# Optimization experiments

Measured on AMD Instinct MI355X. Metric: run time of the kernel, lower is better.

## Reference

```python
import jax, jax.numpy as jnp
import numpy as np

EPS = 1e-08
BASE_CR = 0.5
MIN_CR = 0.1


def _layernorm(h, g, b, eps=1e-5):
    m = jnp.mean(h, axis=-1, keepdims=True)
    v = jnp.mean((h - m) ** 2, axis=-1, keepdims=True)
    return (h - m) * jax.lax.rsqrt(v + eps) * g + b


def _normalize(h, eps=1e-12):
    n = jnp.sqrt(jnp.sum(h * h, axis=-1, keepdims=True))
    return h / jnp.maximum(n, eps)


def _conv1d(h, w, b):
    # h: [B,S,D], w: [K,I,O] (WIO), cross-correlation, SAME padding (torch Conv1d padding=1, k=3)
    y = jax.lax.conv_general_dilated(h, w, window_strides=(1,), padding='SAME',
                                     dimension_numbers=('NWC', 'WIO', 'NWC'))
    return y + b


def setup_inputs() -> dict:
    key = jax.random.key(0)
    ks = jax.random.split(key, 8)
    V, L, D, B, S = 50257, 2048, 1024, 8, 2048
    inp = {
        'x': jax.random.randint(ks[0], (B, S), 0, V),
        'token_emb': jax.random.normal(ks[1], (V, D), jnp.float32) * 0.02,
        'pos_emb': jax.random.normal(ks[2], (L, D), jnp.float32) * 0.02,
        'conv1_w': jax.random.normal(ks[3], (3, D, D), jnp.float32) * 0.025,
        'conv1_b': jnp.zeros((D,), jnp.float32),
        'conv2_w': jax.random.normal(ks[4], (3, D, D), jnp.float32) * 0.025,
        'conv2_b': jnp.zeros((D,), jnp.float32),
        'proj_w': jax.random.normal(ks[5], (D, D), jnp.float32) * 0.03,
        'proj_b': jnp.zeros((D,), jnp.float32),
        'ph_w': jax.random.normal(ks[6], (D, D), jnp.float32) * 0.03,
        'ph_b': jnp.zeros((D,), jnp.float32),
        'ln_g': jnp.ones((D,), jnp.float32),
        'ln_b': jnp.zeros((D,), jnp.float32),
    }
    return inp


def reference(x, token_emb, pos_emb, conv1_w, conv1_b, conv2_w, conv2_b,
              proj_w, proj_b, ph_w, ph_b, ln_g, ln_b):
    B, S = x.shape
    # token + position embedding
    h = token_emb[x] + pos_emb[:S][None, :, :]                 # [B,S,D]
    # two conv1d + gelu (exact erf, matching torch F.gelu default)
    h = jax.nn.gelu(_conv1d(h, conv1_w, conv1_b), approximate=False)
    h = jax.nn.gelu(_conv1d(h, conv2_w, conv2_b), approximate=False)
    h = _layernorm(h, ln_g, ln_b)
    # dropout is identity in eval mode
    # S is a power of two -> next_power_of_two(S) == S, no padding
    x_fft = jnp.fft.fft(h, axis=1)                              # [B,S,D] complex64
    magnitude = jnp.abs(x_fft)
    thresh = 0.1 * jnp.max(magnitude, axis=1, keepdims=True)
    complexity = jnp.mean((magnitude > thresh).astype(jnp.float32), axis=(1, 2))  # [B]
    cr = jnp.clip(BASE_CR * (1.0 - complexity), MIN_CR, 1.0)
    N = jnp.clip((cr * S).astype(jnp.int32), 1, S)              # [B] kept coefficients
    # vectorized ragged masking (replaces per-sample python loop/scatter)
    mask = (jnp.arange(S)[None, :] < N[:, None]).astype(jnp.float32)   # [B,S]
    x_fft_c = x_fft * mask[:, :, None]
    x_ifft_raw = jnp.fft.ifft(x_fft_c, n=S, axis=1).real        # [B,S,D]
    proj_out = x_ifft_raw @ proj_w + proj_b
    x_ifft = _layernorm(proj_out, ln_g, ln_b)
    recon_target = proj_out                                     # same proj of same ifft
    # loss
    cos_sim = jnp.sum(_normalize(x_ifft) * _normalize(recon_target), axis=-1)
    cos_sim = jnp.clip(cos_sim, -1.0 + EPS, 1.0 - EPS)
    d = x_ifft - recon_target
    l1 = jnp.where(jnp.abs(d) < 1.0, 0.5 * d * d, jnp.abs(d) - 0.5)    # smooth_l1, beta=1
    proj_x = x_ifft @ ph_w + ph_b
    proj_t = recon_target @ ph_w + ph_b
    sem = jnp.mean((_normalize(proj_x) - _normalize(proj_t)) ** 2, axis=-1)  # [B,S]
    combined = 0.6 * jnp.mean(1.0 - cos_sim) + 0.2 * jnp.mean(l1, axis=-1) + 0.2 * sem
    loss = jnp.sum(combined * mask) / (jnp.sum(mask) + EPS)
    return (x_ifft, loss)
```

## Files before the change

### kernel.cpp

```cpp
#include <hip/hip_runtime.h>
#include <math.h>

#define S_LEN 2048
#define D_DIM 1024
#define B_BATCH 8
#define R_ROWS (B_BATCH * S_LEN)
#define BD_ROWS (B_BATCH * D_DIM)
#define PAD_ROWS 2050

typedef unsigned short u16;
typedef unsigned int u32;
typedef __attribute__((ext_vector_type(8))) short bf16x8;
typedef __attribute__((ext_vector_type(4))) float f32x4;

__device__ __forceinline__ u16 f2bf(float f) {
    u32 x = __float_as_uint(f);
    u32 r = (x + 0x7fffu + ((x >> 16) & 1u)) >> 16;
    return (u16)r;
}
__device__ __forceinline__ float bf2f(u16 u) {
    return __uint_as_float(((u32)u) << 16);
}
__device__ __forceinline__ float gelu_exact(float x) {
    return 0.5f * x * (1.0f + erff(x * 0.70710678118654752f));
}
__device__ __forceinline__ int dr4(int v) {
    v = __brev((unsigned)v) >> 22;
    return ((v & 0x155) << 1) | ((v >> 1) & 0x155);
}
#define PIDX(i) ((i) + ((i) >> 5))

#define GLDS(gsrc, ldst)                                                                   \
    __builtin_amdgcn_global_load_lds(                                                      \
        (const __attribute__((address_space(1))) u32*)(gsrc),                              \
        (__attribute__((address_space(3))) u32*)(ldst), 16, 0, 0)

#define WAIT_LGKM0 do { asm volatile("s_waitcnt lgkmcnt(0)" ::: "memory");                 \
                        __builtin_amdgcn_sched_barrier(0); } while (0)
#define WAIT_VM(n)   do { asm volatile("s_waitcnt vmcnt(" #n ")" ::: "memory");            \
                          __builtin_amdgcn_sched_barrier(0); } while (0)

__global__ __launch_bounds__(256) void zero_pads(u16* __restrict__ P0, u16* __restrict__ P1)
{
    const int bid = blockIdx.x;
    u16* P = (bid >= 16) ? P1 : P0;
    const int ridx = bid & 15;
    const int b = ridx >> 1;
    const size_t row = (size_t)b * PAD_ROWS + (size_t)(ridx & 1) * (PAD_ROWS - 1);
    ((uint2*)(P + row * D_DIM))[threadIdx.x] = make_uint2(0u, 0u);
}

__global__ __launch_bounds__(256) void wconv(const float* __restrict__ W, u16* __restrict__ WT)
{
    __shared__ float t[32][33];
    const int tap = blockIdx.z;
    const int n0 = blockIdx.x * 32, k0 = blockIdx.y * 32;
    const int tx = threadIdx.x, ty = threadIdx.y;
    const float* ip = W + (size_t)tap * D_DIM * D_DIM;
    u16* op = WT + (size_t)tap * D_DIM * D_DIM;
#pragma unroll
    for (int u = 0; u < 4; u++)
        t[ty + u * 8][tx] = ip[(size_t)(k0 + ty + u * 8) * D_DIM + n0 + tx];
    __syncthreads();
#pragma unroll
    for (int u = 0; u < 4; u++)
        op[(size_t)(n0 + ty + u * 8) * D_DIM + k0 + tx] = f2bf(t[tx][ty + u * 8]);
}

__global__ __launch_bounds__(256) void wconv_scale(
    const float* __restrict__ W, const float* __restrict__ g, u16* __restrict__ WT2)
{
    __shared__ float t[32][33];
    const int n0 = blockIdx.x * 32, k0 = blockIdx.y * 32;
    const int tx = threadIdx.x, ty = threadIdx.y;
#pragma unroll
    for (int u = 0; u < 4; u++)
        t[ty + u * 8][tx] = W[(size_t)(k0 + ty + u * 8) * D_DIM + n0 + tx];
    __syncthreads();
    const float gk = g[k0 + tx];
#pragma unroll
    for (int u = 0; u < 4; u++)
        WT2[(size_t)(n0 + ty + u * 8) * D_DIM + k0 + tx] = f2bf(t[tx][ty + u * 8] * gk);
}

__global__ __launch_bounds__(256) void gemv_ph(
    const u16* __restrict__ WTph, const float* __restrict__ g,
    const float* __restrict__ lnb, const float* __restrict__ phb,
    float* __restrict__ vg, float* __restrict__ c0)
{
    const int wid = threadIdx.x >> 6, lane = threadIdx.x & 63;
    const int n = blockIdx.x * 4 + wid;
    const u16* wrow = WTph + ((size_t)n << 10) + lane * 16;
    float sg = 0.f, sb = 0.f;
#pragma unroll
    for (int h = 0; h < 2; h++) {
        uint4 w = *(const uint4*)(wrow + h * 8);
        float wv[8];
        wv[0] = bf2f((u16)(w.x & 0xffff)); wv[1] = bf2f((u16)(w.x >> 16));
        wv[2] = bf2f((u16)(w.y & 0xffff)); wv[3] = bf2f((u16)(w.y >> 16));
        wv[4] = bf2f((u16)(w.z & 0xffff)); wv[5] = bf2f((u16)(w.z >> 16));
        wv[6] = bf2f((u16)(w.w & 0xffff)); wv[7] = bf2f((u16)(w.w >> 16));
        const int kb = lane * 16 + h * 8;
        float4 g0 = *(const float4*)(g + kb), g1 = *(const float4*)(g + kb + 4);
        float4 b0 = *(const float4*)(lnb + kb), b1 = *(const float4*)(lnb + kb + 4);
        sg += wv[0]*g0.x + wv[1]*g0.y + wv[2]*g0.z + wv[3]*g0.w
            + wv[4]*g1.x + wv[5]*g1.y + wv[6]*g1.z + wv[7]*g1.w;
        sb += wv[0]*b0.x + wv[1]*b0.y + wv[2]*b0.z + wv[3]*b0.w
            + wv[4]*b1.x + wv[5]*b1.y + wv[6]*b1.z + wv[7]*b1.w;
    }
#pragma unroll
    for (int off = 32; off > 0; off >>= 1) {
        sg += __shfl_xor(sg, off);
        sb += __shfl_xor(sb, off);
    }
    if (lane == 0) { vg[n] = sg; c0[n] = sb + phb[n]; }
}

__global__ __launch_bounds__(256) void emb_kernel(
    const int* __restrict__ x, const float* __restrict__ tok,
    const float* __restrict__ pos, u16* __restrict__ P0)
{
    const int row = blockIdx.x;
    const int tid = threadIdx.x;
    const int t = x[row];
    const int s = row & (S_LEN - 1);
    const int b = row >> 11;
    float4 a = ((const float4*)(tok + (size_t)t * D_DIM))[tid];
    float4 p = ((const float4*)(pos + (size_t)s * D_DIM))[tid];
    uint2 v;
    v.x = (u32)f2bf(a.x + p.x) | ((u32)f2bf(a.y + p.y) << 16);
    v.y = (u32)f2bf(a.z + p.z) | ((u32)f2bf(a.w + p.w) << 16);
    ((uint2*)(P0 + ((size_t)b * PAD_ROWS + 1 + s) * D_DIM))[tid] = v;
}

__global__ __launch_bounds__(512, 2) void gemm_8ph(
    const u16* __restrict__ A, const u16* __restrict__ WT,
    const float* __restrict__ bias,
    float* __restrict__ outF, u16* __restrict__ outB,
    int ntaps, int doGelu, int aPadded, int outBPadded)
{
    __shared__ u16 As[2][2][8192];
    __shared__ u16 Bs[2][2][8192];
    const int tid = threadIdx.x;
    const int wid = tid >> 6, lane = tid & 63;
    const int wm = wid >> 2, wn = wid & 3;
    const int l15 = lane & 15, l4 = lane >> 4;
    const int flat = blockIdx.y * 4 + blockIdx.x;
    const int xcd = flat & 7;
    const int ii = flat >> 3;
    const int by = xcd * 8 + (ii >> 2);
    const int bx = ii & 3;
    const int row0 = by * 256;
    const int col0 = bx * 256;
    const int b = row0 >> 11;
    const int srow0 = row0 & (S_LEN - 1);
    const int nt = ntaps * 16;
    const int NI = nt >> 1;

    const int stR = tid >> 2;
    const int stKc = (((tid & 3) ^ ((tid >> 2) & 3)) << 3);
    const int ldsOff = tid * 16;
    const int swz4 = ((l4 ^ (l15 & 3)) << 4);

#define STAGE_A(T_, s_) do {                                                               \
        const int tap_ = (T_) >> 4;                                                        \
        const int kb_ = ((T_) & 15) * 64 + (s_) * 32 + stKc;                               \
        const size_t ar_ = (aPadded ? (size_t)(b * PAD_ROWS + srow0 + tap_)                \
                                    : (size_t)row0);                                       \
        GLDS(A + ((ar_ + stR) << 10) + kb_,                                                \
             (char*)&As[(T_) & 1][s_][0] + ldsOff);                                        \
        GLDS(A + ((ar_ + stR + 128) << 10) + kb_,                                          \
             (char*)&As[(T_) & 1][s_][0] + ldsOff + 8192);                                 \
    } while (0)
#define STAGE_B(T_, s_) do {                                                               \
        const int tap_ = (T_) >> 4;                                                        \
        const int kb_ = ((T_) & 15) * 64 + (s_) * 32 + stKc;                               \
        const u16* wp_ = WT + ((size_t)tap_ << 20) + ((size_t)(col0 + stR) << 10) + kb_;   \
        GLDS(wp_, (char*)&Bs[(T_) & 1][s_][0] + ldsOff);                                   \
        GLDS(wp_ + (size_t)(128 << 10), (char*)&Bs[(T_) & 1][s_][0] + ldsOff + 8192);      \
    } while (0)
#define RD_A(dst_, buf_, s_, mih_) do {                                                    \
        const char* p_ = (const char*)&As[buf_][s_][0]                                     \
                         + (size_t)(wm * 128 + (mih_) * 64 + l15) * 64 + swz4;             \
        dst_[0] = *(const bf16x8*)(p_);                                                    \
        dst_[1] = *(const bf16x8*)(p_ + 1024);                                             \
        dst_[2] = *(const bf16x8*)(p_ + 2048);                                             \
        dst_[3] = *(const bf16x8*)(p_ + 3072);                                             \
    } while (0)
#define RD_B(dst_, buf_, s_) do {                                                          \
        const char* p_ = (const char*)&Bs[buf_][s_][0]                                     \
                         + (size_t)(wn * 64 + l15) * 64 + swz4;                            \
        dst_[0] = *(const bf16x8*)(p_);                                                    \
        dst_[1] = *(const bf16x8*)(p_ + 1024);                                             \
        dst_[2] = *(const bf16x8*)(p_ + 2048);                                             \
        dst_[3] = *(const bf16x8*)(p_ + 3072);                                             \
    } while (0)
#define MF(mih_, av_, bv_) do {                                                            \
        __builtin_amdgcn_s_setprio(1);                                                     \
        _Pragma("unroll")                                                                  \
        for (int mi_ = 0; mi_ < 4; mi_++)                                                  \
            _Pragma("unroll")                                                              \
            for (int ni_ = 0; ni_ < 4; ni_++)                                              \
                acc[(mih_) * 4 + mi_][ni_] = __builtin_amdgcn_mfma_f32_16x16x32_bf16(      \
                    av_[mi_], bv_[ni_], acc[(mih_) * 4 + mi_][ni_], 0, 0, 0);              \
        __builtin_amdgcn_s_setprio(0);                                                     \
    } while (0)
#define BAR __builtin_amdgcn_s_barrier()

    f32x4 acc[8][4];
#pragma unroll
    for (int m = 0; m < 8; m++)
#pragma unroll
        for (int n = 0; n < 4; n++) acc[m][n] = (f32x4){0.f, 0.f, 0.f, 0.f};

    STAGE_A(0, 0); STAGE_B(0, 0);
    STAGE_A(0, 1); STAGE_B(0, 1);
    STAGE_A(1, 0); STAGE_B(1, 0);
    WAIT_VM(4);
    BAR;

    for (int i = 0; i < NI; ++i) {
        const int o = 2 * i + 1;
        const int e2 = 2 * i + 2, o2 = 2 * i + 3;
        const bool last = (i == NI - 1);
        bf16x8 a[4], bv[4];
        RD_A(a, 0, 0, 0); RD_B(bv, 0, 0);
        STAGE_A(o, 1);
        BAR; WAIT_LGKM0;
        MF(0, a, bv);
        BAR;
        RD_A(a, 0, 0, 1);
        STAGE_B(o, 1);
        BAR; WAIT_LGKM0;
        MF(1, a, bv);
        BAR;
        RD_A(a, 0, 1, 0); RD_B(bv, 0, 1);
        if (!last) STAGE_A(e2, 0);
        BAR; WAIT_LGKM0;
        MF(0, a, bv);
        BAR;
        RD_A(a, 0, 1, 1);
        if (!last) STAGE_B(e2, 0);
        BAR; WAIT_LGKM0;
        MF(1, a, bv);
        if (last) { WAIT_VM(0); } else { WAIT_VM(4); }
        BAR;
        RD_A(a, 1, 0, 0); RD_B(bv, 1, 0);
        if (!last) STAGE_A(e2, 1);
        BAR; WAIT_LGKM0;
        MF(0, a, bv);
        BAR;
        RD_A(a, 1, 0, 1);
        if (!last) STAGE_B(e2, 1);
        BAR; WAIT_LGKM0;
        MF(1, a, bv);
        BAR;
        RD_A(a, 1, 1, 0); RD_B(bv, 1, 1);
        if (!last) STAGE_A(o2, 0);
        BAR; WAIT_LGKM0;
        MF(0, a, bv);
        BAR;
        RD_A(a, 1, 1, 1);
        if (!last) STAGE_B(o2, 0);
        BAR; WAIT_LGKM0;
        MF(1, a, bv);
        if (!last) { WAIT_VM(4); }
        BAR;
    }
#undef STAGE_A
#undef STAGE_B
#undef RD_A
#undef RD_B
#undef MF
#undef BAR

    float bb[4];
#pragma unroll
    for (int ni = 0; ni < 4; ni++) bb[ni] = bias[col0 + wn * 64 + ni * 16 + l15];

#pragma unroll
    for (int mi = 0; mi < 8; mi++) {
#pragma unroll
        for (int ni = 0; ni < 4; ni++) {
#pragma unroll
            for (int reg = 0; reg < 4; reg++) {
                const int row = row0 + wm * 128 + mi * 16 + l4 * 4 + reg;
                const int col = col0 + wn * 64 + ni * 16 + l15;
                float v = acc[mi][ni][reg] + bb[ni];
                if (doGelu) v = gelu_exact(v);
                if (outF) outF[(size_t)row * D_DIM + col] = v;
                if (outB) {
                    const size_t orow = outBPadded
                        ? ((size_t)(row >> 11) * PAD_ROWS + 1 + (size_t)(row & (S_LEN - 1)))
                        : (size_t)row;
                    outB[orow * D_DIM + col] = f2bf(v);
                }
            }
        }
    }
}

__global__ __launch_bounds__(256, 3) void phstats_mfma(
    const u16* __restrict__ R, const u16* __restrict__ WT1, const u16* __restrict__ WT2,
    const float* __restrict__ phb, const float* __restrict__ vg, const float* __restrict__ c0,
    const float2* __restrict__ stats2,
    float* __restrict__ Sxx, float* __restrict__ Stt, float* __restrict__ Sxt)
{
    __shared__ u16 Abuf[128 * 32];
    __shared__ u16 B1buf[64 * 32];
    __shared__ u16 B2buf[64 * 32];
    const int tid = threadIdx.x;
    const int wid = tid >> 6, lane = tid & 63;
    const int wr = wid >> 1, wc = wid & 1;
    const int flat = blockIdx.y * 16 + blockIdx.x;
    const int xcd = flat & 7;
    const int i = flat >> 3;
    const int by = xcd * 16 + (i >> 4);
    const int bx = i & 15;
    const int col0 = bx * 64;
    const int row0 = by * 128;
    const int l15 = lane & 15, l4 = lane >> 4;

    f32x4 acc1[4][2], acc2[4][2];
#pragma unroll
    for (int m = 0; m < 4; m++)
#pragma unroll
        for (int n = 0; n < 2; n++) {
            acc1[m][n] = (f32x4){0.f, 0.f, 0.f, 0.f};
            acc2[m][n] = (f32x4){0.f, 0.f, 0.f, 0.f};
        }

    for (int k0 = 0; k0 < D_DIM; k0 += 32) {
#pragma unroll
        for (int c = 0; c < 2; c++) {
            const int off = (wid + c * 4) * 1024 + lane * 16;
            const int r = off >> 6;
            const int cb = off & 63;
            GLDS(R + ((size_t)(row0 + r) << 10) + (size_t)(k0 + (cb >> 1)),
                 (char*)Abuf + off);
        }
        {
            const int off = wid * 1024 + lane * 16;
            const int r = off >> 6;
            const int cb = off & 63;
            GLDS(WT1 + ((size_t)(col0 + r) << 10) + (size_t)(k0 + (cb >> 1)),
                 (char*)B1buf + off);
            GLDS(WT2 + ((size_t)(col0 + r) << 10) + (size_t)(k0 + (cb >> 1)),
                 (char*)B2buf + off);
        }
        __syncthreads();
        bf16x8 af[4], b1f[2], b2f[2];
#pragma unroll
        for (int mi = 0; mi < 4; mi++)
            af[mi] = *(const bf16x8*)&Abuf[(wr * 64 + mi * 16 + l15) * 32 + l4 * 8];
#pragma unroll
        for (int ni = 0; ni < 2; ni++) {
            b1f[ni] = *(const bf16x8*)&B1buf[(wc * 32 + ni * 16 + l15) * 32 + l4 * 8];
            b2f[ni] = *(const bf16x8*)&B2buf[(wc * 32 + ni * 16 + l15) * 32 + l4 * 8];
        }
#pragma unroll
        for (int mi = 0; mi < 4; mi++)
#pragma unroll
            for (int ni = 0; ni < 2; ni++) {
                acc1[mi][ni] = __builtin_amdgcn_mfma_f32_16x16x32_bf16(
                    af[mi], b1f[ni], acc1[mi][ni], 0, 0, 0);
                acc2[mi][ni] = __builtin_amdgcn_mfma_f32_16x16x32_bf16(
                    af[mi], b2f[ni], acc2[mi][ni], 0, 0, 0);
            }
        __syncthreads();
    }

    float phv[2], vgv[2], c0v[2];
#pragma unroll
    for (int ni = 0; ni < 2; ni++) {
        const int col = col0 + wc * 32 + ni * 16 + l15;
        phv[ni] = phb[col]; vgv[ni] = vg[col]; c0v[ni] = c0[col];
    }
#pragma unroll
    for (int mi = 0; mi < 4; mi++) {
#pragma unroll
        for (int reg = 0; reg < 4; reg++) {
            const int row = row0 + wr * 64 + mi * 16 + l4 * 4 + reg;
            const float2 st = stats2[row];
            const float mrs = st.x * st.y;
            float sxx = 0.f, stt = 0.f, sxt = 0.f;
#pragma unroll
            for (int ni = 0; ni < 2; ni++) {
                float pt = acc1[mi][ni][reg] + phv[ni];
                float px = st.y * acc2[mi][ni][reg] - mrs * vgv[ni] + c0v[ni];
                sxx = fmaf(px, px, sxx);
                stt = fmaf(pt, pt, stt);
                sxt = fmaf(px, pt, sxt);
            }
#pragma unroll
            for (int off = 1; off < 16; off <<= 1) {
                sxx += __shfl_xor(sxx, off);
                stt += __shfl_xor(stt, off);
                sxt += __shfl_xor(sxt, off);
            }
            if (l15 == 0) {
                atomicAdd(&Sxx[row], sxx);
                atomicAdd(&Stt[row], stt);
                atomicAdd(&Sxt[row], sxt);
            }
        }
    }
}

__global__ __launch_bounds__(256) void ln_stats(
    const u16* __restrict__ in, float2* __restrict__ stats)
{
    const int row = blockIdx.x;
    const int tid = threadIdx.x;
    uint2 raw = ((const uint2*)(in + (size_t)row * D_DIM))[tid];
    float v0 = bf2f((u16)(raw.x & 0xffff)), v1 = bf2f((u16)(raw.x >> 16));
    float v2 = bf2f((u16)(raw.y & 0xffff)), v3 = bf2f((u16)(raw.y >> 16));
    float s = v0 + v1 + v2 + v3;
    float s2 = v0 * v0 + v1 * v1 + v2 * v2 + v3 * v3;
#pragma unroll
    for (int off = 32; off > 0; off >>= 1) {
        s += __shfl_xor(s, off);
        s2 += __shfl_xor(s2, off);
    }
    __shared__ float red[8];
    if ((tid & 63) == 0) { red[(tid >> 6) * 2] = s; red[(tid >> 6) * 2 + 1] = s2; }
    __syncthreads();
    if (tid == 0) {
        s = red[0] + red[2] + red[4] + red[6];
        s2 = red[1] + red[3] + red[5] + red[7];
        const float m = s * (1.0f / D_DIM);
        const float var = s2 * (1.0f / D_DIM) - m * m;
        stats[row] = make_float2(m, rsqrtf(var + 1e-5f));
    }
}

__global__ __launch_bounds__(256) void transposeLN(
    const u16* __restrict__ in, const float2* __restrict__ stats,
    const float* __restrict__ g, const float* __restrict__ beta,
    float* __restrict__ out)
{
    __shared__ float t[32][33];
    const int b = blockIdx.z;
    const int n0 = blockIdx.x * 32, m0 = blockIdx.y * 32;
    const int tx = threadIdx.x, ty = threadIdx.y;
    const u16* ip = in + (size_t)b * S_LEN * D_DIM;
    float* op = out + (size_t)b * S_LEN * D_DIM;
#pragma unroll
    for (int u = 0; u < 4; u++)
        t[ty + u * 8][tx] = bf2f(ip[(size_t)(m0 + ty + u * 8) * D_DIM + n0 + tx]);
    __syncthreads();
    const float2 st = stats[b * S_LEN + m0 + tx];
#pragma unroll
    for (int u = 0; u < 4; u++) {
        const int d = n0 + ty + u * 8;
        const float val = (t[tx][ty + u * 8] - st.x) * st.y * g[d] + beta[d];
        op[(size_t)d * S_LEN + m0 + tx] = val;
    }
}

__global__ __launch_bounds__(256) void fft_fwd(
    const float* __restrict__ in, float2* __restrict__ X, int* __restrict__ counts)
{
    __shared__ float re[1056], im[1056], twr[1024], twi[1024];
    __shared__ float redf[4];
    __shared__ int redi[4];
    const int tid = threadIdx.x;
    const int row = blockIdx.x;
    const float2* src = (const float2*)(in + (size_t)row * S_LEN);
#pragma unroll
    for (int u = 0; u < 4; u++) {
        int e = tid + u * 256;
        float ang = -3.14159265358979f * (float)e * (1.0f / 512.0f);
        float sn, cs; __sincosf(ang, &sn, &cs);
        twr[e] = cs; twi[e] = sn;
    }
#pragma unroll
    for (int u = 0; u < 4; u++) {
        int t = tid + u * 256;
        float2 z = src[t];
        int p = PIDX(dr4(t));
        re[p] = z.x; im[p] = z.y;
    }
    __syncthreads();
#pragma unroll
    for (int s = 1; s <= 5; ++s) {
        const int mq = 1 << (2 * (s - 1));
        const int fsh = 2 * (5 - s);
        const int j = tid & (mq - 1);
        const int g = tid >> (2 * (s - 1));
        const int i0 = (g << (2 * s)) + j;
        const int e1 = j << fsh;
        const int p0 = PIDX(i0), p1 = PIDX(i0 + mq), p2 = PIDX(i0 + 2 * mq), p3 = PIDX(i0 + 3 * mq);
        float a0r = re[p0], a0i = im[p0];
        float a1r = re[p1], a1i = im[p1];
        float a2r = re[p2], a2i = im[p2];
        float a3r = re[p3], a3i = im[p3];
        float w1r = twr[e1], w1i = twi[e1];
        float w2r = twr[2 * e1], w2i = twi[2 * e1];
        float w3r = twr[3 * e1], w3i = twi[3 * e1];
        float b1r = a1r * w1r - a1i * w1i, b1i = a1r * w1i + a1i * w1r;
        float b2r = a2r * w2r - a2i * w2i, b2i = a2r * w2i + a2i * w2r;
        float b3r = a3r * w3r - a3i * w3i, b3i = a3r * w3i + a3i * w3r;
        float t0r = a0r + b2r, t0i = a0i + b2i;
        float t1r = a0r - b2r, t1i = a0i - b2i;
        float t2r = b1r + b3r, t2i = b1i + b3i;
        float t3r = b1r - b3r, t3i = b1i - b3i;
        re[p0] = t0r + t2r; im[p0] = t0i + t2i;
        re[p2] = t0r - t2r; im[p2] = t0i - t2i;
        re[p1] = t1r + t3i; im[p1] = t1i - t3r;
        re[p3] = t1r - t3i; im[p3] = t1i + t3r;
        __syncthreads();
    }
    float2* dst = X + (size_t)row * 1024;
    float mag[4];
    float xtra = 0.0f;
    float lmax = 0.0f;
#pragma unroll
    for (int u = 0; u < 4; u++) {
        int k = tid + u * 256;
        int mk = (1024 - k) & 1023;
        float rk = re[PIDX(k)], ik = im[PIDX(k)];
        float rm = re[PIDX(mk)], imm = im[PIDX(mk)];
        float er = 0.5f * (rk + rm);
        float ei = 0.5f * (ik - imm);
        float orr = 0.5f * (ik + imm);
        float oii = -0.5f * (rk - rm);
        float ang = -3.14159265358979f * (float)k * (1.0f / 1024.0f);
        float sn, cs; __sincosf(ang, &sn, &cs);
        float xr = er + orr * cs - oii * sn;
        float xi = ei + orr * sn + oii * cs;
        dst[k] = make_float2(xr, xi);
        float m2 = xr * xr + xi * xi;
        mag[u] = m2;
        lmax = fmaxf(lmax, m2);
        if (k == 0) {
            float x1024 = re[PIDX(0)] - im[PIDX(0)];
            xtra = x1024 * x1024;
            lmax = fmaxf(lmax, xtra);
        }
    }
#pragma unroll
    for (int off = 32; off > 0; off >>= 1) lmax = fmaxf(lmax, __shfl_xor(lmax, off));
    if ((tid & 63) == 0) redf[tid >> 6] = lmax;
    __syncthreads();
    const float bmax = fmaxf(fmaxf(redf[0], redf[1]), fmaxf(redf[2], redf[3]));
    const float thr = 0.01f * bmax;
    int lc = 0;
#pragma unroll
    for (int u = 0; u < 4; u++) {
        int k = tid + u * 256;
        lc += (mag[u] > thr) ? ((k == 0) ? 1 : 2) : 0;
    }
    if (tid == 0) lc += (xtra > thr) ? 1 : 0;
#pragma unroll
    for (int off = 32; off > 0; off >>= 1) lc += __shfl_xor(lc, off);
    if ((tid & 63) == 0) redi[tid >> 6] = lc;
    __syncthreads();
    if (tid == 0)
        atomicAdd(&counts[(row >> 10) * 64 + (row & 63)],
                  redi[0] + redi[1] + redi[2] + redi[3]);
}

__global__ void calc_n(const int* __restrict__ counts, int* __restrict__ Ndev)
{
    const int t = threadIdx.x;
    for (int b = 0; b < B_BATCH; b++) {
        int c = counts[b * 64 + t];
#pragma unroll
        for (int off = 32; off > 0; off >>= 1) c += __shfl_xor(c, off);
        if (t == 0) {
            float cf = (float)c * (1.0f / 2097152.0f);
            float cr = 0.5f * (1.0f - cf);
            cr = fminf(fmaxf(cr, 0.1f), 1.0f);
            int n = (int)(cr * 2048.0f);
            n = n < 1 ? 1 : (n > S_LEN ? S_LEN : n);
            Ndev[b] = n;
        }
    }
}

__global__ __launch_bounds__(256) void fft_inv(
    const float2* __restrict__ X, const int* __restrict__ Ndev,
    u16* __restrict__ outb)
{
    __shared__ float re[1056], im[1056], twr[1024], twi[1024];
    const int tid = threadIdx.x;
    const int row = blockIdx.x;
    const int Nb = Ndev[row >> 10];
    const float2* src = X + (size_t)row * 1024;
#pragma unroll
    for (int u = 0; u < 4; u++) {
        int e = tid + u * 256;
        float ang = 3.14159265358979f * (float)e * (1.0f / 512.0f);
        float sn, cs; __sincosf(ang, &sn, &cs);
        twr[e] = cs; twi[e] = sn;
    }
#pragma unroll
    for (int u = 0; u < 4; u++) {
        int k = tid + u * 256;
        float Ar = 0.f, Ai = 0.f, Br = 0.f, Bi = 0.f;
        if (k == 0) {
            float2 h = src[0];
            Ar = h.x; Ai = h.y;
        } else {
            if (k < Nb) { float2 h = src[k]; Ar = 0.5f * h.x; Ai = 0.5f * h.y; }
            int km = 1024 - k;
            if (km < Nb) { float2 h = src[km]; Br = 0.5f * h.x; Bi = -0.5f * h.y; }
        }
        float ang = 3.14159265358979f * (float)k * (1.0f / 1024.0f);
        float sn, cs; __sincosf(ang, &sn, &cs);
        float drr = Ar - Br, dri = Ai - Bi;
        float Dr = drr * cs - dri * sn;
        float Di = drr * sn + dri * cs;
        float Cr = (Ar + Br) - Di;
        float Ci = (Ai + Bi) + Dr;
        int p = PIDX(dr4(k));
        re[p] = Cr; im[p] = Ci;
    }
    __syncthreads();
#pragma unroll
    for (int s = 1; s <= 4; ++s) {
        const int mq = 1 << (2 * (s - 1));
        const int fsh = 2 * (5 - s);
        const int j = tid & (mq - 1);
        const int g = tid >> (2 * (s - 1));
        const int i0 = (g << (2 * s)) + j;
        const int e1 = j << fsh;
        const int p0 = PIDX(i0), p1 = PIDX(i0 + mq), p2 = PIDX(i0 + 2 * mq), p3 = PIDX(i0 + 3 * mq);
        float a0r = re[p0], a0i = im[p0];
        float a1r = re[p1], a1i = im[p1];
        float a2r = re[p2], a2i = im[p2];
        float a3r = re[p3], a3i = im[p3];
        float w1r = twr[e1], w1i = twi[e1];
        float w2r = twr[2 * e1], w2i = twi[2 * e1];
        float w3r = twr[3 * e1], w3i = twi[3 * e1];
        float b1r = a1r * w1r - a1i * w1i, b1i = a1r * w1i + a1i * w1r;
        float b2r = a2r * w2r - a2i * w2i, b2i = a2r * w2i + a2i * w2r;
        float b3r = a3r * w3r - a3i * w3i, b3i = a3r * w3i + a3i * w3r;
        float t0r = a0r + b2r, t0i = a0i + b2i;
        float t1r = a0r - b2r, t1i = a0i - b2i;
        float t2r = b1r + b3r, t2i = b1i + b3i;
        float t3r = b1r - b3r, t3i = b1i - b3i;
        re[p0] = t0r + t2r; im[p0] = t0i + t2i;
        re[p2] = t0r - t2r; im[p2] = t0i - t2i;
        re[p1] = t1r - t3i; im[p1] = t1i + t3r;
        re[p3] = t1r + t3i; im[p3] = t1i - t3r;
        __syncthreads();
    }
    {
        const int j = tid;
        const int e1 = j;
        const int p0 = PIDX(j), p1 = PIDX(j + 256), p2 = PIDX(j + 512), p3 = PIDX(j + 768);
        float a0r = re[p0], a0i = im[p0];
        float a1r = re[p1], a1i = im[p1];
        float a2r = re[p2], a2i = im[p2];
        float a3r = re[p3], a3i = im[p3];
        float w1r = twr[e1], w1i = twi[e1];
        float w2r = twr[2 * e1], w2i = twi[2 * e1];
        float w3r = twr[3 * e1], w3i = twi[3 * e1];
        float b1r = a1r * w1r - a1i * w1i, b1i = a1r * w1i + a1i * w1r;
        float b2r = a2r * w2r - a2i * w2i, b2i = a2r * w2i + a2i * w2r;
        float b3r = a3r * w3r - a3i * w3i, b3i = a3r * w3i + a3i * w3r;
        float t0r = a0r + b2r, t0i = a0i + b2i;
        float t1r = a0r - b2r, t1i = a0i - b2i;
        float t2r = b1r + b3r, t2i = b1i + b3i;
        float t3r = b1r - b3r, t3i = b1i - b3i;
        const float sc = 1.0f / 2048.0f;
        u32* dst = (u32*)(outb + (size_t)row * S_LEN);
        dst[j]       = (u32)f2bf((t0r + t2r) * sc) | ((u32)f2bf((t0i + t2i) * sc) << 16);
        dst[j + 256] = (u32)f2bf((t1r - t3i) * sc) | ((u32)f2bf((t1i + t3r) * sc) << 16);
        dst[j + 512] = (u32)f2bf((t0r - t2r) * sc) | ((u32)f2bf((t0i - t2i) * sc) << 16);
        dst[j + 768] = (u32)f2bf((t1r + t3i) * sc) | ((u32)f2bf((t1i - t3r) * sc) << 16);
    }
}

__global__ __launch_bounds__(256) void transpose_bb(
    const u16* __restrict__ in, u16* __restrict__ out, int M, int N)
{
    __shared__ u16 t[32][33];
    const int b = blockIdx.z;
    const int n0 = blockIdx.x * 32, m0 = blockIdx.y * 32;
    const int tx = threadIdx.x, ty = threadIdx.y;
    const u16* ip = in + (size_t)b * M * N;
    u16* op = out + (size_t)b * M * N;
#pragma unroll
    for (int u = 0; u < 4; u++)
        t[ty + u * 8][tx] = ip[(size_t)(m0 + ty + u * 8) * N + n0 + tx];
    __syncthreads();
#pragma unroll
    for (int u = 0; u < 4; u++)
        op[(size_t)(n0 + ty + u * 8) * M + m0 + tx] = t[tx][ty + u * 8];
}

__global__ __launch_bounds__(256) void ln_loss(
    const float* __restrict__ in, const float* __restrict__ g,
    const float* __restrict__ beta, float* __restrict__ outF,
    float2* __restrict__ stats2,
    float* __restrict__ rowA, float* __restrict__ rowL1)
{
    const int row = blockIdx.x;
    const int tid = threadIdx.x;
    float4 v = ((const float4*)(in + (size_t)row * D_DIM))[tid];
    float s = v.x + v.y + v.z + v.w;
    float s2 = v.x * v.x + v.y * v.y + v.z * v.z + v.w * v.w;
#pragma unroll
    for (int off = 32; off > 0; off >>= 1) {
        s += __shfl_xor(s, off);
        s2 += __shfl_xor(s2, off);
    }
    __shared__ float red[8];
    if ((tid & 63) == 0) { red[(tid >> 6) * 2] = s; red[(tid >> 6) * 2 + 1] = s2; }
    __syncthreads();
    s = red[0] + red[2] + red[4] + red[6];
    s2 = red[1] + red[3] + red[5] + red[7];
    const float m = s * (1.0f / D_DIM);
    const float var = s2 * (1.0f / D_DIM) - m * m;
    const float rs = rsqrtf(var + 1e-5f);
    float4 gg = ((const float4*)g)[tid];
    float4 bb = ((const float4*)beta)[tid];
    float4 o;
    o.x = (v.x - m) * rs * gg.x + bb.x;
    o.y = (v.y - m) * rs * gg.y + bb.y;
    o.z = (v.z - m) * rs * gg.z + bb.z;
    o.w = (v.w - m) * rs * gg.w + bb.w;
    ((float4*)(outF + (size_t)row * D_DIM))[tid] = o;

    float xx = o.x * o.x + o.y * o.y + o.z * o.z + o.w * o.w;
    float rr = v.x * v.x + v.y * v.y + v.z * v.z + v.w * v.w;
    float xr = o.x * v.x + o.y * v.y + o.z * v.z + o.w * v.w;
    float l1 = 0.f;
    {
        float d, ad;
        d = o.x - v.x; ad = fabsf(d); l1 += (ad < 1.0f) ? 0.5f * d * d : ad - 0.5f;
        d = o.y - v.y; ad = fabsf(d); l1 += (ad < 1.0f) ? 0.5f * d * d : ad - 0.5f;
        d = o.z - v.z; ad = fabsf(d); l1 += (ad < 1.0f) ? 0.5f * d * d : ad - 0.5f;
        d = o.w - v.w; ad = fabsf(d); l1 += (ad < 1.0f) ? 0.5f * d * d : ad - 0.5f;
    }
#pragma unroll
    for (int off = 32; off > 0; off >>= 1) {
        xx += __shfl_xor(xx, off); rr += __shfl_xor(rr, off);
        xr += __shfl_xor(xr, off); l1 += __shfl_xor(l1, off);
    }
    __shared__ float red2[4][4];
    __syncthreads();
    if ((tid & 63) == 0) {
        int w = tid >> 6;
        red2[w][0] = xx; red2[w][1] = rr; red2[w][2] = xr; red2[w][3] = l1;
    }
    __syncthreads();
    if (tid == 0) {
        stats2[row] = make_float2(m, rs);
        xx = red2[0][0] + red2[1][0] + red2[2][0] + red2[3][0];
        rr = red2[0][1] + red2[1][1] + red2[2][1] + red2[3][1];
        xr = red2[0][2] + red2[1][2] + red2[2][2] + red2[3][2];
        l1 = red2[0][3] + red2[1][3] + red2[2][3] + red2[3][3];
        float nx = fmaxf(sqrtf(xx), 1e-12f);
        float nr = fmaxf(sqrtf(rr), 1e-12f);
        float cs = xr / (nx * nr);
        cs = fminf(fmaxf(cs, -1.0f + 1e-8f), 1.0f - 1e-8f);
        rowA[row] = 1.0f - cs;
        rowL1[row] = l1;
    }
}

__global__ __launch_bounds__(1024) void final_loss(
    const float* __restrict__ rowA, const float* __restrict__ rowL1,
    const float* __restrict__ Sxx, const float* __restrict__ Stt,
    const float* __restrict__ Sxt,
    const int* __restrict__ Ndev, float* __restrict__ out)
{
    const int tid = threadIdx.x;
    float sa = 0.f, sb = 0.f;
#pragma unroll
    for (int i = 0; i < 16; i++) {
        int r = tid + i * 1024;
        sa += rowA[r];
        int b = r >> 11, s = r & (S_LEN - 1);
        if (s < Ndev[b]) {
            float sx = Sxx[r], st = Stt[r], sxtv = Sxt[r];
            float nxx = fmaxf(sqrtf(sx), 1e-12f);
            float ntt = fmaxf(sqrtf(st), 1e-12f);
            float sem = (sx / (nxx * nxx) + st / (ntt * ntt)
                         - 2.0f * sxtv / (nxx * ntt)) * (1.0f / D_DIM);
            sb += 0.2f * (rowL1[r] * (1.0f / D_DIM)) + 0.2f * sem;
        }
    }
#pragma unroll
    for (int off = 32; off > 0; off >>= 1) {
        sa += __shfl_xor(sa, off);
        sb += __shfl_xor(sb, off);
    }
    __shared__ float ra[16], rb[16];
    if ((tid & 63) == 0) { ra[tid >> 6] = sa; rb[tid >> 6] = sb; }
    __syncthreads();
    if (tid == 0) {
        float A = 0.f, Bs = 0.f;
#pragma unroll
        for (int i = 0; i < 16; i++) { A += ra[i]; Bs += rb[i]; }
        int K = 0;
        for (int b = 0; b < B_BATCH; b++) K += Ndev[b];
        float Kf = (float)K;
        float M = A * (1.0f / 16384.0f);
        out[(size_t)R_ROWS * D_DIM] = (0.6f * M * Kf + Bs) / (Kf + 1e-8f);
    }
}

extern "C" void kernel_launch(void* const* d_in, const int* in_sizes, int n_in,
                              void* d_out, int out_size, void* d_ws, size_t ws_size,
                              hipStream_t stream)
{
    (void)in_sizes; (void)n_in; (void)out_size; (void)ws_size;
    const int*   x       = (const int*)  d_in[0];
    const float* tok     = (const float*)d_in[1];
    const float* pos     = (const float*)d_in[2];
    const float* conv1_w = (const float*)d_in[3];
    const float* conv1_b = (const float*)d_in[4];
    const float* conv2_w = (const float*)d_in[5];
    const float* conv2_b = (const float*)d_in[6];
    const float* proj_w  = (const float*)d_in[7];
    const float* proj_b  = (const float*)d_in[8];
    const float* ph_w    = (const float*)d_in[9];
    const float* ph_b    = (const float*)d_in[10];
    const float* ln_g    = (const float*)d_in[11];
    const float* ln_b    = (const float*)d_in[12];
    float* out = (float*)d_out;

    char* ws = (char*)d_ws;
    int*    counts = (int*)(ws);
    int*    Ndev   = (int*)(ws + 2048);
    float2* stats  = (float2*)(ws + 4096);
    float2* stats2 = (float2*)(ws + 135168);
    float*  Sxx    = (float*)(ws + 266240);
    float*  Stt    = (float*)(ws + 331776);
    float*  Sxt    = (float*)(ws + 397312);
    float*  rowA   = (float*)(ws + 462848);
    float*  rowL1  = (float*)(ws + 528384);
    float*  vg     = (float*)(ws + 593920);
    float*  c0     = (float*)(ws + 598016);
    const size_t MB = 1ull << 20;
    u16*   WT   = (u16*)(ws + 1 * MB);
    u16*   WT2  = WT;
    u16*   P0   = (u16*)(ws + 17 * MB);
    u16*   P1   = (u16*)(ws + 50 * MB);
    float* F32A = (float*)(ws + 83 * MB);
    float* F32B = (float*)(ws + 148 * MB);

    hipMemsetAsync(ws, 0, MB, stream);
    zero_pads<<<32, 256, 0, stream>>>(P0, P1);
    wconv<<<dim3(32, 32, 3), dim3(32, 8), 0, stream>>>(conv1_w, WT);
    wconv<<<dim3(32, 32, 3), dim3(32, 8), 0, stream>>>(conv2_w, WT + 3u * (1u << 20));
    wconv<<<dim3(32, 32, 1), dim3(32, 8), 0, stream>>>(proj_w, WT + 6u * (1u << 20));
    wconv<<<dim3(32, 32, 1), dim3(32, 8), 0, stream>>>(ph_w, WT + 7u * (1u << 20));
    gemv_ph<<<256, 256, 0, stream>>>(WT + 7u * (1u << 20), ln_g, ln_b, ph_b, vg, c0);
    emb_kernel<<<R_ROWS, 256, 0, stream>>>(x, tok, pos, P0);
    gemm_8ph<<<dim3(4, 64), 512, 0, stream>>>(P0, WT, conv1_b,
                                              nullptr, P1, 3, 1, 1, 1);
    wconv_scale<<<dim3(32, 32, 1), dim3(32, 8), 0, stream>>>(ph_w, ln_g, WT2);
    gemm_8ph<<<dim3(4, 64), 512, 0, stream>>>(P1, WT + 3u * (1u << 20), conv2_b,
                                              nullptr, P0, 3, 1, 1, 0);
    ln_stats<<<R_ROWS, 256, 0, stream>>>(P0, stats);
    transposeLN<<<dim3(32, 64, 8), dim3(32, 8), 0, stream>>>(P0, stats, ln_g, ln_b, F32B);
    fft_fwd<<<BD_ROWS, 256, 0, stream>>>(F32B, (float2*)F32A, counts);
    calc_n<<<1, 64, 0, stream>>>(counts, Ndev);
    fft_inv<<<BD_ROWS, 256, 0, stream>>>((const float2*)F32A, Ndev, P1);
    transpose_bb<<<dim3(64, 32, 8), dim3(32, 8), 0, stream>>>(P1, P0, D_DIM, S_LEN);
    gemm_8ph<<<dim3(4, 64), 512, 0, stream>>>(P0, WT + 6u * (1u << 20), proj_b,
                                              F32A, P1, 1, 0, 0, 0);
    ln_loss<<<R_ROWS, 256, 0, stream>>>(F32A, ln_g, ln_b, out, stats2, rowA, rowL1);
    phstats_mfma<<<dim3(16, 128), 256, 0, stream>>>(P1, WT + 7u * (1u << 20), WT2,
                                                    ph_b, vg, c0, stats2, Sxx, Stt, Sxt);
    final_loss<<<1, 1024, 0, stream>>>(rowA, rowL1, Sxx, Stt, Sxt, Ndev, out);
}
```

Measured before the change: 627.5 us.

## Interleave ph weights and reuse 8-phase GEMM pipeline for ph stats kernel

Builds one interleaved weight matrix holding each ph_w column and its ln_g-scaled copy in adjacent rows. The ph stats GEMM then runs as a single 16384x2048x1024 GEMM on the pipelined 256x256 tile scheme of gemm_8ph, replacing the smaller 128x64 kernel that kept two accumulator sets. Paired outputs are combined with a lane shuffle and every sum is halved because each pair is counted twice. The LDS swizzle pattern changes in both GEMMs, gemv_ph now reads the interleaved rows, and the separate wconv for ph_w is dropped.

```diff
diff --git a/kernel.cpp b/kernel.cpp
--- a/kernel.cpp
+++ b/kernel.cpp
@@ -67,8 +67,8 @@
         op[(size_t)(n0 + ty + u * 8) * D_DIM + k0 + tx] = f2bf(t[tx][ty + u * 8]);
 }
 
-__global__ __launch_bounds__(256) void wconv_scale(
-    const float* __restrict__ W, const float* __restrict__ g, u16* __restrict__ WT2)
+__global__ __launch_bounds__(256) void wconv_inter(
+    const float* __restrict__ W, const float* __restrict__ g, u16* __restrict__ WTI)
 {
     __shared__ float t[32][33];
     const int n0 = blockIdx.x * 32, k0 = blockIdx.y * 32;
@@ -79,34 +79,41 @@
     __syncthreads();
     const float gk = g[k0 + tx];
 #pragma unroll
-    for (int u = 0; u < 4; u++)
-        WT2[(size_t)(n0 + ty + u * 8) * D_DIM + k0 + tx] = f2bf(t[tx][ty + u * 8] * gk);
+    for (int u = 0; u < 4; u++) {
+        const int n = n0 + ty + u * 8;
+        const float w = t[tx][ty + u * 8];
+        WTI[((size_t)(2 * n) << 10) + k0 + tx] = f2bf(w);
+        WTI[((size_t)(2 * n + 1) << 10) + k0 + tx] = f2bf(w * gk);
+    }
 }
 
 __global__ __launch_bounds__(256) void gemv_ph(
-    const u16* __restrict__ WTph, const float* __restrict__ g,
-    const float* __restrict__ lnb, const float* __restrict__ phb,
-    float* __restrict__ vg, float* __restrict__ c0)
+    const u16* __restrict__ WTI, const float* __restrict__ lnb,
+    const float* __restrict__ phb, float* __restrict__ vg, float* __restrict__ c0)
 {
     const int wid = threadIdx.x >> 6, lane = threadIdx.x & 63;
     const int n = blockIdx.x * 4 + wid;
-    const u16* wrow = WTph + ((size_t)n << 10) + lane * 16;
-    float sg = 0.f, sb = 0.f;
+    const u16* r0 = WTI + ((size_t)(2 * n) << 10) + lane * 16;
+    const u16* r1 = WTI + ((size_t)(2 * n + 1) << 10) + lane * 16;
+    float sb = 0.f, sg = 0.f;
 #pragma unroll
     for (int h = 0; h < 2; h++) {
-        uint4 w = *(const uint4*)(wrow + h * 8);
-        float wv[8];
-        wv[0] = bf2f((u16)(w.x & 0xffff)); wv[1] = bf2f((u16)(w.x >> 16));
-        wv[2] = bf2f((u16)(w.y & 0xffff)); wv[3] = bf2f((u16)(w.y >> 16));
-        wv[4] = bf2f((u16)(w.z & 0xffff)); wv[5] = bf2f((u16)(w.z >> 16));
-        wv[6] = bf2f((u16)(w.w & 0xffff)); wv[7] = bf2f((u16)(w.w >> 16));
+        uint4 w0 = *(const uint4*)(r0 + h * 8);
+        uint4 w1 = *(const uint4*)(r1 + h * 8);
+        float a[8], b8[8];
+        a[0] = bf2f((u16)(w0.x & 0xffff)); a[1] = bf2f((u16)(w0.x >> 16));
+        a[2] = bf2f((u16)(w0.y & 0xffff)); a[3] = bf2f((u16)(w0.y >> 16));
+        a[4] = bf2f((u16)(w0.z & 0xffff)); a[5] = bf2f((u16)(w0.z >> 16));
+        a[6] = bf2f((u16)(w0.w & 0xffff)); a[7] = bf2f((u16)(w0.w >> 16));
+        b8[0] = bf2f((u16)(w1.x & 0xffff)); b8[1] = bf2f((u16)(w1.x >> 16));
+        b8[2] = bf2f((u16)(w1.y & 0xffff)); b8[3] = bf2f((u16)(w1.y >> 16));
+        b8[4] = bf2f((u16)(w1.z & 0xffff)); b8[5] = bf2f((u16)(w1.z >> 16));
+        b8[6] = bf2f((u16)(w1.w & 0xffff)); b8[7] = bf2f((u16)(w1.w >> 16));
         const int kb = lane * 16 + h * 8;
-        float4 g0 = *(const float4*)(g + kb), g1 = *(const float4*)(g + kb + 4);
-        float4 b0 = *(const float4*)(lnb + kb), b1 = *(const float4*)(lnb + kb + 4);
-        sg += wv[0]*g0.x + wv[1]*g0.y + wv[2]*g0.z + wv[3]*g0.w
-            + wv[4]*g1.x + wv[5]*g1.y + wv[6]*g1.z + wv[7]*g1.w;
-        sb += wv[0]*b0.x + wv[1]*b0.y + wv[2]*b0.z + wv[3]*b0.w
-            + wv[4]*b1.x + wv[5]*b1.y + wv[6]*b1.z + wv[7]*b1.w;
+        float4 l0 = *(const float4*)(lnb + kb), l1 = *(const float4*)(lnb + kb + 4);
+        sb += a[0]*l0.x + a[1]*l0.y + a[2]*l0.z + a[3]*l0.w
+            + a[4]*l1.x + a[5]*l1.y + a[6]*l1.z + a[7]*l1.w;
+        sg += b8[0] + b8[1] + b8[2] + b8[3] + b8[4] + b8[5] + b8[6] + b8[7];
     }
 #pragma unroll
     for (int off = 32; off > 0; off >>= 1) {
@@ -158,9 +165,9 @@
     const int NI = nt >> 1;
 
     const int stR = tid >> 2;
-    const int stKc = (((tid & 3) ^ ((tid >> 2) & 3)) << 3);
+    const int stKc = (((tid & 3) ^ ((tid >> 3) & 3)) << 3);
     const int ldsOff = tid * 16;
-    const int swz4 = ((l4 ^ (l15 & 3)) << 4);
+    const int swz4 = ((l4 ^ ((l15 >> 1) & 3)) << 4);
 
 #define STAGE_A(T_, s_) do {                                                               \
         const int tap_ = (T_) >> 4;                                                        \
@@ -268,11 +275,6 @@
         BAR;
     }
 #undef STAGE_A
-#undef STAGE_B
-#undef RD_A
-#undef RD_B
-#undef MF
-#undef BAR
 
     float bb[4];
 #pragma unroll
@@ -300,97 +302,140 @@
     }
 }
 
-__global__ __launch_bounds__(256, 3) void phstats_mfma(
-    const u16* __restrict__ R, const u16* __restrict__ WT1, const u16* __restrict__ WT2,
-    const float* __restrict__ phb, const float* __restrict__ vg, const float* __restrict__ c0,
-    const float2* __restrict__ stats2,
+__global__ __launch_bounds__(512, 2) void phstats_8ph(
+    const u16* __restrict__ A, const u16* __restrict__ WTI,
+    const float* __restrict__ phb, const float* __restrict__ vg,
+    const float* __restrict__ c0, const float2* __restrict__ stats2,
     float* __restrict__ Sxx, float* __restrict__ Stt, float* __restrict__ Sxt)
 {
-    __shared__ u16 Abuf[128 * 32];
-    __shared__ u16 B1buf[64 * 32];
-    __shared__ u16 B2buf[64 * 32];
+    __shared__ u16 As[2][2][8192];
+    __shared__ u16 Bs[2][2][8192];
     const int tid = threadIdx.x;
     const int wid = tid >> 6, lane = tid & 63;
-    const int wr = wid >> 1, wc = wid & 1;
-    const int flat = blockIdx.y * 16 + blockIdx.x;
+    const int wm = wid >> 2, wn = wid & 3;
+    const int l15 = lane & 15, l4 = lane >> 4;
+    const int flat = blockIdx.y * 8 + blockIdx.x;
     const int xcd = flat & 7;
-    const int i = flat >> 3;
-    const int by = xcd * 16 + (i >> 4);
-    const int bx = i & 15;
-    const int col0 = bx * 64;
-    const int row0 = by * 128;
-    const int l15 = lane & 15, l4 = lane >> 4;
-
-    f32x4 acc1[4][2], acc2[4][2];
-#pragma unroll
-    for (int m = 0; m < 4; m++)
-#pragma unroll
-        for (int n = 0; n < 2; n++) {
-            acc1[m][n] = (f32x4){0.f, 0.f, 0.f, 0.f};
-            acc2[m][n] = (f32x4){0.f, 0.f, 0.f, 0.f};
-        }
-
-    for (int k0 = 0; k0 < D_DIM; k0 += 32) {
-#pragma unroll
-        for (int c = 0; c < 2; c++) {
-            const int off = (wid + c * 4) * 1024 + lane * 16;
-            const int r = off >> 6;
-            const int cb = off & 63;
-            GLDS(R + ((size_t)(row0 + r) << 10) + (size_t)(k0 + (cb >> 1)),
-                 (char*)Abuf + off);
-        }
-        {
-            const int off = wid * 1024 + lane * 16;
-            const int r = off >> 6;
-            const int cb = off & 63;
-            GLDS(WT1 + ((size_t)(col0 + r) << 10) + (size_t)(k0 + (cb >> 1)),
-                 (char*)B1buf + off);
-            GLDS(WT2 + ((size_t)(col0 + r) << 10) + (size_t)(k0 + (cb >> 1)),
-                 (char*)B2buf + off);
-        }
-        __syncthreads();
-        bf16x8 af[4], b1f[2], b2f[2];
-#pragma unroll
-        for (int mi = 0; mi < 4; mi++)
-            af[mi] = *(const bf16x8*)&Abuf[(wr * 64 + mi * 16 + l15) * 32 + l4 * 8];
-#pragma unroll
-        for (int ni = 0; ni < 2; ni++) {
-            b1f[ni] = *(const bf16x8*)&B1buf[(wc * 32 + ni * 16 + l15) * 32 + l4 * 8];
-            b2f[ni] = *(const bf16x8*)&B2buf[(wc * 32 + ni * 16 + l15) * 32 + l4 * 8];
-        }
-#pragma unroll
-        for (int mi = 0; mi < 4; mi++)
-#pragma unroll
-            for (int ni = 0; ni < 2; ni++) {
-                acc1[mi][ni] = __builtin_amdgcn_mfma_f32_16x16x32_bf16(
-                    af[mi], b1f[ni], acc1[mi][ni], 0, 0, 0);
-                acc2[mi][ni] = __builtin_amdgcn_mfma_f32_16x16x32_bf16(
-                    af[mi], b2f[ni], acc2[mi][ni], 0, 0, 0);
-            }
-        __syncthreads();
-    }
-
-    float phv[2], vgv[2], c0v[2];
-#pragma unroll
-    for (int ni = 0; ni < 2; ni++) {
-        const int col = col0 + wc * 32 + ni * 16 + l15;
-        phv[ni] = phb[col]; vgv[ni] = vg[col]; c0v[ni] = c0[col];
-    }
-#pragma unroll
-    for (int mi = 0; mi < 4; mi++) {
+    const int ii = flat >> 3;
+    const int by = xcd * 8 + (ii >> 3);
+    const int bx = ii & 7;
+    const int row0 = by * 256;
+    const int col0 = bx * 256;
+    const int NI = 8;
+
+    const int stR = tid >> 2;
+    const int stKc = (((tid & 3) ^ ((tid >> 3) & 3)) << 3);
+    const int ldsOff = tid * 16;
+    const int swz4 = ((l4 ^ ((l15 >> 1) & 3)) << 4);
+
+#define STAGE_A(T_, s_) do {                                                               \
+        const int kb_ = ((T_) & 15) * 64 + (s_) * 32 + stKc;                               \
+        GLDS(A + (((size_t)row0 + stR) << 10) + kb_,                                       \
+             (char*)&As[(T_) & 1][s_][0] + ldsOff);                                        \
+        GLDS(A + (((size_t)row0 + stR + 128) << 10) + kb_,                                 \
+             (char*)&As[(T_) & 1][s_][0] + ldsOff + 8192);                                 \
+    } while (0)
+#define STAGE_BI(T_, s_) do {                                                              \
+        const int kb_ = ((T_) & 15) * 64 + (s_) * 32 + stKc;                               \
+        const u16* wp_ = WTI + ((size_t)(col0 + stR) << 10) + kb_;                         \
+        GLDS(wp_, (char*)&Bs[(T_) & 1][s_][0] + ldsOff);                                   \
+        GLDS(wp_ + (size_t)(128 << 10), (char*)&Bs[(T_) & 1][s_][0] + ldsOff + 8192);      \
+    } while (0)
+
+    f32x4 acc[8][4];
+#pragma unroll
+    for (int m = 0; m < 8; m++)
+#pragma unroll
+        for (int n = 0; n < 4; n++) acc[m][n] = (f32x4){0.f, 0.f, 0.f, 0.f};
+
+    STAGE_A(0, 0); STAGE_BI(0, 0);
+    STAGE_A(0, 1); STAGE_BI(0, 1);
+    STAGE_A(1, 0); STAGE_BI(1, 0);
+    WAIT_VM(4);
+    BAR;
+
+    for (int i = 0; i < NI; ++i) {
+        const int o = 2 * i + 1;
+        const int e2 = 2 * i + 2, o2 = 2 * i + 3;
+        const bool last = (i == NI - 1);
+        bf16x8 a[4], bv[4];
+        RD_A(a, 0, 0, 0); RD_B(bv, 0, 0);
+        STAGE_A(o, 1);
+        BAR; WAIT_LGKM0;
+        MF(0, a, bv);
+        BAR;
+        RD_A(a, 0, 0, 1);
+        STAGE_BI(o, 1);
+        BAR; WAIT_LGKM0;
+        MF(1, a, bv);
+        BAR;
+        RD_A(a, 0, 1, 0); RD_B(bv, 0, 1);
+        if (!last) STAGE_A(e2, 0);
+        BAR; WAIT_LGKM0;
+        MF(0, a, bv);
+        BAR;
+        RD_A(a, 0, 1, 1);
+        if (!last) STAGE_BI(e2, 0);
+        BAR; WAIT_LGKM0;
+        MF(1, a, bv);
+        if (last) { WAIT_VM(0); } else { WAIT_VM(4); }
+        BAR;
+        RD_A(a, 1, 0, 0); RD_B(bv, 1, 0);
+        if (!last) STAGE_A(e2, 1);
+        BAR; WAIT_LGKM0;
+        MF(0, a, bv);
+        BAR;
+        RD_A(a, 1, 0, 1);
+        if (!last) STAGE_BI(e2, 1);
+        BAR; WAIT_LGKM0;
+        MF(1, a, bv);
+        BAR;
+        RD_A(a, 1, 1, 0); RD_B(bv, 1, 1);
+        if (!last) STAGE_A(o2, 0);
+        BAR; WAIT_LGKM0;
+        MF(0, a, bv);
+        BAR;
+        RD_A(a, 1, 1, 1);
+        if (!last) STAGE_BI(o2, 0);
+        BAR; WAIT_LGKM0;
+        MF(1, a, bv);
+        if (!last) { WAIT_VM(4); }
+        BAR;
+    }
+#undef STAGE_A
+#undef STAGE_BI
+#undef RD_A
+#undef RD_B
+#undef MF
+#undef BAR
+
+    float phv[4], vgv[4], c0v[4];
+#pragma unroll
+    for (int ni = 0; ni < 4; ni++) {
+        const int col = col0 + wn * 64 + ni * 16 + l15;
+        const int j = col >> 1;
+        phv[ni] = phb[j]; vgv[ni] = vg[j]; c0v[ni] = c0[j];
+    }
+    const bool odd = (l15 & 1) != 0;
+#pragma unroll
+    for (int mi = 0; mi < 8; mi++) {
 #pragma unroll
         for (int reg = 0; reg < 4; reg++) {
-            const int row = row0 + wr * 64 + mi * 16 + l4 * 4 + reg;
+            const int row = row0 + wm * 128 + mi * 16 + l4 * 4 + reg;
             const float2 st = stats2[row];
             const float mrs = st.x * st.y;
             float sxx = 0.f, stt = 0.f, sxt = 0.f;
 #pragma unroll
-            for (int ni = 0; ni < 2; ni++) {
-                float pt = acc1[mi][ni][reg] + phv[ni];
-                float px = st.y * acc2[mi][ni][reg] - mrs * vgv[ni] + c0v[ni];
+            for (int ni = 0; ni < 4; ni++) {
+                const float raw = acc[mi][ni][reg];
+                const float val = odd ? (st.y * raw - mrs * vgv[ni] + c0v[ni])
+                                      : (raw + phv[ni]);
+                const float par = __shfl_xor(val, 1);
+                const float pt = odd ? par : val;
+                const float px = odd ? val : par;
+                stt = fmaf(pt, pt, stt);
                 sxx = fmaf(px, px, sxx);
-                stt = fmaf(pt, pt, stt);
-                sxt = fmaf(px, pt, sxt);
+                sxt = fmaf(pt, px, sxt);
             }
 #pragma unroll
             for (int off = 1; off < 16; off <<= 1) {
@@ -399,9 +444,9 @@
                 sxt += __shfl_xor(sxt, off);
             }
             if (l15 == 0) {
-                atomicAdd(&Sxx[row], sxx);
-                atomicAdd(&Stt[row], stt);
-                atomicAdd(&Sxt[row], sxt);
+                atomicAdd(&Sxx[row], 0.5f * sxx);
+                atomicAdd(&Stt[row], 0.5f * stt);
+                atomicAdd(&Sxt[row], 0.5f * sxt);
             }
         }
     }
@@ -839,7 +884,7 @@
     float*  c0     = (float*)(ws + 598016);
     const size_t MB = 1ull << 20;
     u16*   WT   = (u16*)(ws + 1 * MB);
-    u16*   WT2  = WT;
+    u16*   WTI  = WT;
     u16*   P0   = (u16*)(ws + 17 * MB);
     u16*   P1   = (u16*)(ws + 50 * MB);
     float* F32A = (float*)(ws + 83 * MB);
@@ -850,12 +895,11 @@
     wconv<<<dim3(32, 32, 3), dim3(32, 8), 0, stream>>>(conv1_w, WT);
     wconv<<<dim3(32, 32, 3), dim3(32, 8), 0, stream>>>(conv2_w, WT + 3u * (1u << 20));
     wconv<<<dim3(32, 32, 1), dim3(32, 8), 0, stream>>>(proj_w, WT + 6u * (1u << 20));
-    wconv<<<dim3(32, 32, 1), dim3(32, 8), 0, stream>>>(ph_w, WT + 7u * (1u << 20));
-    gemv_ph<<<256, 256, 0, stream>>>(WT + 7u * (1u << 20), ln_g, ln_b, ph_b, vg, c0);
     emb_kernel<<<R_ROWS, 256, 0, stream>>>(x, tok, pos, P0);
     gemm_8ph<<<dim3(4, 64), 512, 0, stream>>>(P0, WT, conv1_b,
                                               nullptr, P1, 3, 1, 1, 1);
-    wconv_scale<<<dim3(32, 32, 1), dim3(32, 8), 0, stream>>>(ph_w, ln_g, WT2);
+    wconv_inter<<<dim3(32, 32, 1), dim3(32, 8), 0, stream>>>(ph_w, ln_g, WTI);
+    gemv_ph<<<256, 256, 0, stream>>>(WTI, ln_b, ph_b, vg, c0);
     gemm_8ph<<<dim3(4, 64), 512, 0, stream>>>(P1, WT + 3u * (1u << 20), conv2_b,
                                               nullptr, P0, 3, 1, 1, 0);
     ln_stats<<<R_ROWS, 256, 0, stream>>>(P0, stats);
@@ -867,7 +911,7 @@
     gemm_8ph<<<dim3(4, 64), 512, 0, stream>>>(P0, WT + 6u * (1u << 20), proj_b,
                                               F32A, P1, 1, 0, 0, 0);
     ln_loss<<<R_ROWS, 256, 0, stream>>>(F32A, ln_g, ln_b, out, stats2, rowA, rowL1);
-    phstats_mfma<<<dim3(16, 128), 256, 0, stream>>>(P1, WT + 7u * (1u << 20), WT2,
-                                                    ph_b, vg, c0, stats2, Sxx, Stt, Sxt);
+    phstats_8ph<<<dim3(8, 64), 512, 0, stream>>>(P1, WTI, ph_b, vg, c0, stats2,
+                                                 Sxx, Stt, Sxt);
     final_loss<<<1, 1024, 0, stream>>>(rowA, rowL1, Sxx, Stt, Sxt, Ndev, out);
 }
```

Measured after the change: 603.2 us. 3.9% less time.
